# Performance work log

Measured on AMD Instinct MI355X. Metric: run time of the kernel, lower is better.

The kernel has to match this reference:

```python
import jax, jax.numpy as jnp
import numpy as np
import math

B, L, D = 2, 2048, 1024
H = 16
DH = D // H  # 64
XPOS_SCALE_BASE = 512.0
THETA = 10000.0


def setup_inputs() -> dict:
    key = jax.random.key(0)
    ks = jax.random.split(key, 9)
    s = 0.02  # keep logits in a sane range like trained weights
    return {
        "x": jax.random.normal(ks[0], (B, L, D), dtype=jnp.float32),
        "Wq": jax.random.normal(ks[1], (D, D), dtype=jnp.float32) * s,
        "bq": jax.random.normal(ks[2], (D,), dtype=jnp.float32) * s,
        "Wk": jax.random.normal(ks[3], (D, D), dtype=jnp.float32) * s,
        "bk": jax.random.normal(ks[4], (D,), dtype=jnp.float32) * s,
        "Wv": jax.random.normal(ks[5], (D, D), dtype=jnp.float32) * s,
        "bv": jax.random.normal(ks[6], (D,), dtype=jnp.float32) * s,
        "Wo": jax.random.normal(ks[7], (D, D), dtype=jnp.float32) * s,
        "bo": jax.random.normal(ks[8], (D,), dtype=jnp.float32) * s,
    }


def _rotate_half(t):
    # pairwise interleaved rotation, as in rotary_embedding_torch
    t1 = t[..., 0::2]
    t2 = t[..., 1::2]
    return jnp.stack([-t2, t1], axis=-1).reshape(t.shape)


def _xpos_rotate(q, k):
    # q, k: [B, H, L, DH]; xPos rotary embedding (use_xpos=True)
    seq = q.shape[2]
    half = jnp.arange(0, DH, 2, dtype=jnp.float32)
    inv_freq = 1.0 / (THETA ** (half / DH))            # [DH/2]
    t = jnp.arange(seq, dtype=jnp.float32)             # [L]
    freqs = t[:, None] * inv_freq[None, :]             # [L, DH/2]
    freqs = jnp.repeat(freqs, 2, axis=-1)              # [L, DH] interleaved
    # xPos length-extrapolatable scale
    scale_vec = (half + 0.4 * DH) / (1.4 * DH)         # [DH/2]
    power = (t - seq // 2) / XPOS_SCALE_BASE           # [L]
    scale = scale_vec[None, :] ** power[:, None]       # [L, DH/2]
    scale = jnp.repeat(scale, 2, axis=-1)              # [L, DH]
    cos = jnp.cos(freqs)
    sin = jnp.sin(freqs)
    q_out = q * (cos * scale) + _rotate_half(q) * (sin * scale)
    k_out = k * (cos / scale) + _rotate_half(k) * (sin / scale)
    return q_out, k_out


def reference(x, Wq, bq, Wk, bk, Wv, bv, Wo, bo):
    b, l, d = x.shape
    # projections; note source swaps names: v_mat <- k-proj, k_mat <- v-proj
    q = (x @ Wq.T + bq).reshape(b, l, H, DH).transpose(0, 2, 1, 3)  # [b,h,l,dh]
    v = (x @ Wk.T + bk).reshape(b, l, H, DH).transpose(0, 2, 1, 3)
    k = (x @ Wv.T + bv).reshape(b, l, H, DH).transpose(0, 2, 1, 3)
    q, k = _xpos_rotate(q, k)
    # source divides by sqrt(Dh * num_heads) == sqrt(dim)
    scores = jnp.einsum("bhqd,bhkd->bhqk", q, k) / math.sqrt(d)
    weights = jax.nn.softmax(scores, axis=-1)
    inter = jnp.einsum("bhqk,bhkd->bhqd", weights, v)
    inter = inter.transpose(0, 2, 1, 3).reshape(b, l, d)
    return inter @ Wo.T + bo
```

## Files before the change

kernel.cpp:

```cpp
#include <hip/hip_runtime.h>
#include <math.h>

#define NB 2
#define NL 2048
#define ND 1024
#define NH 16
#define NDH 64
#define NBL 4096

typedef __attribute__((ext_vector_type(4)))  float f32x4;
typedef __attribute__((ext_vector_type(16))) float f32x16;
typedef __attribute__((ext_vector_type(8)))  short s16x8;
typedef __attribute__((ext_vector_type(4)))  short s16x4;

#define LOG2E 1.44269504088896f

__device__ __forceinline__ float fexp2(float x){
#if __has_builtin(__builtin_amdgcn_exp2f)
  return __builtin_amdgcn_exp2f(x);
#else
  return exp2f(x);
#endif
}

__device__ __forceinline__ unsigned short f2bf(float f){
  unsigned int u = __float_as_uint(f);
  u += 0x7FFF + ((u >> 16) & 1);
  return (unsigned short)(u >> 16);
}

__device__ __forceinline__ unsigned int pk2bf(float lo, float hi){
  return __builtin_amdgcn_perm(__float_as_uint(hi) + 0x8000u,
                               __float_as_uint(lo) + 0x8000u, 0x07060302u);
}

__global__ void cvt_all(const float* __restrict__ x,
                        const float* __restrict__ wq, const float* __restrict__ wk,
                        const float* __restrict__ wv, const float* __restrict__ wo,
                        unsigned short* __restrict__ xb,
                        unsigned short* __restrict__ wqb, unsigned short* __restrict__ wkb,
                        unsigned short* __restrict__ wvb, unsigned short* __restrict__ wob){
  int i = blockIdx.x * blockDim.x + threadIdx.x;
  const float* s; unsigned short* d; int off;
  if (i < (1<<20)) { s = x; d = xb; off = i; }
  else {
    int j = i - (1<<20); int w = j >> 18; off = j & ((1<<18)-1);
    s = (w==0)?wq:(w==1)?wk:(w==2)?wv:wo;
    d = (w==0)?wqb:(w==1)?wkb:(w==2)?wvb:wob;
  }
  float4 f = reinterpret_cast<const float4*>(s)[off];
  ushort4 r; r.x=f2bf(f.x); r.y=f2bf(f.y); r.z=f2bf(f.z); r.w=f2bf(f.w);
  reinterpret_cast<ushort4*>(d)[off] = r;
}

__global__ void rope_tables(float2* __restrict__ qtab, float2* __restrict__ ktab){
  int t = blockIdx.x * blockDim.x + threadIdx.x;
  int l = t >> 5, i = t & 31;
  float half = 2.0f * (float)i;
  float inv_freq = 1.0f / powf(10000.0f, half / 64.0f);
  float fr = (float)l * inv_freq;
  float sv = (half + 0.4f * 64.0f) / (1.4f * 64.0f);
  float pw = ((float)l - 1024.0f) / 512.0f;
  float sc = powf(sv, pw);
  float cs = cosf(fr), sn = sinf(fr);
  qtab[t] = make_float2(cs * sc, sn * sc);
  ktab[t] = make_float2(cs / sc, sn / sc);
}

__device__ __forceinline__ void gemm_core128(
    const unsigned short* __restrict__ A, const unsigned short* __restrict__ W,
    int row0, int col0,
    unsigned short (&As)[128][32], unsigned short (&Bs)[128][32],
    f32x4 (&acc)[4][4])
{
  const int tid  = threadIdx.x;
  const int wave = tid >> 6, lane = tid & 63;
  const int m16  = lane & 15, quad = lane >> 4;
  const int mrow = (wave & 1) * 64, ncol = (wave >> 1) * 64;
  const int rA   = lane >> 2, cA = (lane & 3) * 8;

  for (int k0 = 0; k0 < ND; k0 += 32){
    __syncthreads();
#pragma unroll
    for (int i2 = 0; i2 < 2; i2++){
      const int c = wave * 2 + i2;
      const unsigned short* ga = A + (size_t)(row0 + c*16 + rA) * ND + k0 + cA;
      const unsigned short* gb = W + (size_t)(col0 + c*16 + rA) * ND + k0 + cA;
      __builtin_amdgcn_global_load_lds((const __attribute__((address_space(1))) void*)ga,
                                       (__attribute__((address_space(3))) void*)&As[c*16][0], 16, 0, 0);
      __builtin_amdgcn_global_load_lds((const __attribute__((address_space(1))) void*)gb,
                                       (__attribute__((address_space(3))) void*)&Bs[c*16][0], 16, 0, 0);
    }
    __syncthreads();
    s16x8 af[4], bf[4];
#pragma unroll
    for (int mt = 0; mt < 4; mt++) af[mt] = *reinterpret_cast<const s16x8*>(&As[mrow + mt*16 + m16][quad*8]);
#pragma unroll
    for (int nt = 0; nt < 4; nt++) bf[nt] = *reinterpret_cast<const s16x8*>(&Bs[ncol + nt*16 + m16][quad*8]);
#pragma unroll
    for (int mt = 0; mt < 4; mt++)
#pragma unroll
      for (int nt = 0; nt < 4; nt++)
        acc[mt][nt] = __builtin_amdgcn_mfma_f32_16x16x32_bf16(af[mt], bf[nt], acc[mt][nt], 0, 0, 0);
  }
}

__global__ __launch_bounds__(256) void gemm_qkv(
    const unsigned short* __restrict__ A,
    const unsigned short* __restrict__ Wq, const float* __restrict__ bq,
    const unsigned short* __restrict__ Wk, const float* __restrict__ bk,
    const unsigned short* __restrict__ Wv, const float* __restrict__ bv,
    unsigned short* __restrict__ qb, unsigned short* __restrict__ kb,
    unsigned short* __restrict__ vtb,
    const float2* __restrict__ qtab, const float2* __restrict__ ktab)
{
  __shared__ unsigned short As[128][32];
  __shared__ unsigned short Bs[128][32];
  __shared__ unsigned short T[128][72];

  const int mode = blockIdx.z;
  const unsigned short* W = (mode==0) ? Wq : (mode==1) ? Wk : Wv;
  const float* bias       = (mode==0) ? bq : (mode==1) ? bk : bv;

  const int row0 = blockIdx.x * 128, col0 = blockIdx.y * 128;
  f32x4 acc[4][4] = {};
  gemm_core128(A, W, row0, col0, As, Bs, acc);

  const int tid  = threadIdx.x;
  const int wave = tid >> 6, lane = tid & 63;
  const int m16  = lane & 15, quad = lane >> 4;
  const int mrow = (wave & 1) * 64, ncol = (wave >> 1) * 64;

  if (mode == 2){
    const int b = row0 >> 11, l0 = row0 & (NL - 1);
#pragma unroll
    for (int h2 = 0; h2 < 2; h2++){
      __syncthreads();
      if ((wave >> 1) == h2){
#pragma unroll
        for (int mt = 0; mt < 4; mt++)
#pragma unroll
          for (int nt = 0; nt < 4; nt++)
#pragma unroll
            for (int r = 0; r < 4; r++){
              int lrow = mrow + mt*16 + quad*4 + r;
              int dh   = nt*16 + m16;
              T[lrow][dh] = f2bf(acc[mt][nt][r] + bias[col0 + h2*64 + dh]);
            }
      }
      __syncthreads();
      const int bh = b * NH + (col0 >> 6) + h2;
#pragma unroll
      for (int j4 = 0; j4 < 4; j4++){
        int c = tid * 4 + j4;
        int d = c >> 4, seg = (c & 15) * 8;
        unsigned short tmp[8];
#pragma unroll
        for (int jj = 0; jj < 8; jj++) tmp[jj] = T[seg + jj][d];
        *reinterpret_cast<uint4*>(vtb + (size_t)(bh * NDH + d) * NL + l0 + seg) =
            *reinterpret_cast<uint4*>(tmp);
      }
    }
  } else {
    const float qscale = (mode == 0) ? (0.03125f * LOG2E) : 1.0f;
    const float2* tab  = (mode == 0) ? qtab : ktab;
    unsigned short* dst = (mode == 0) ? qb : kb;
#pragma unroll
    for (int mt = 0; mt < 4; mt++)
#pragma unroll
      for (int nt = 0; nt < 4; nt++)
#pragma unroll
        for (int r = 0; r < 4; r++){
          int grow = row0 + mrow + mt*16 + quad*4 + r;
          int gcol = col0 + ncol + nt*16 + m16;
          float v = acc[mt][nt][r] + bias[gcol];
          int b = grow >> 11, l = grow & (NL - 1);
          int h = gcol >> 6, dh = gcol & 63;
          float pv = __shfl_xor(v, 1);
          float2 t = tab[l*32 + (dh >> 1)];
          float rh = (dh & 1) ? pv : -pv;
          float ov = (v * t.x + rh * t.y) * qscale;
          dst[(((size_t)(b * NH + h)) * NL + l) * NDH + dh] = f2bf(ov);
        }
  }
}

__global__ __launch_bounds__(256) void gemm_o(
    const unsigned short* __restrict__ A, const unsigned short* __restrict__ W,
    const float* __restrict__ bias, float* __restrict__ out)
{
  __shared__ unsigned short As[128][32];
  __shared__ unsigned short Bs[64][32];
  const int tid  = threadIdx.x;
  const int wave = tid >> 6, lane = tid & 63;
  const int m16  = lane & 15, quad = lane >> 4;
  const int mrow = (wave & 1) * 64, ncol = (wave >> 1) * 32;
  const int rA   = lane >> 2, cA = (lane & 3) * 8;
  const int row0 = blockIdx.x * 128, col0 = blockIdx.y * 64;

  f32x4 acc[4][2] = {};

  for (int k0 = 0; k0 < ND; k0 += 32){
    __syncthreads();
#pragma unroll
    for (int i3 = 0; i3 < 3; i3++){
      const int c = wave * 3 + i3;
      const unsigned short* g; unsigned short* l;
      if (c < 8){ g = A + (size_t)(row0 + c*16 + rA) * ND + k0 + cA;      l = &As[c*16][0]; }
      else      { g = W + (size_t)(col0 + (c-8)*16 + rA) * ND + k0 + cA;  l = &Bs[(c-8)*16][0]; }
      __builtin_amdgcn_global_load_lds((const __attribute__((address_space(1))) void*)g,
                                       (__attribute__((address_space(3))) void*)l, 16, 0, 0);
    }
    __syncthreads();
    s16x8 af[4], bf[2];
#pragma unroll
    for (int mt = 0; mt < 4; mt++) af[mt] = *reinterpret_cast<const s16x8*>(&As[mrow + mt*16 + m16][quad*8]);
#pragma unroll
    for (int nt = 0; nt < 2; nt++) bf[nt] = *reinterpret_cast<const s16x8*>(&Bs[ncol + nt*16 + m16][quad*8]);
#pragma unroll
    for (int mt = 0; mt < 4; mt++)
#pragma unroll
      for (int nt = 0; nt < 2; nt++)
        acc[mt][nt] = __builtin_amdgcn_mfma_f32_16x16x32_bf16(af[mt], bf[nt], acc[mt][nt], 0, 0, 0);
  }

#pragma unroll
  for (int mt = 0; mt < 4; mt++)
#pragma unroll
    for (int nt = 0; nt < 2; nt++)
#pragma unroll
      for (int r = 0; r < 4; r++){
        int grow = row0 + mrow + mt*16 + quad*4 + r;
        int gcol = col0 + ncol + nt*16 + m16;
        out[(size_t)grow * ND + gcol] = acc[mt][nt][r] + bias[gcol];
      }
}

__global__ __launch_bounds__(256, 2) void attn_kernel(
    const unsigned short* __restrict__ qb,
    const unsigned short* __restrict__ kb,
    const unsigned short* __restrict__ vtb,
    unsigned short* __restrict__ ob)
{
  __shared__ unsigned short Ks[64 * 64];
  __shared__ unsigned short Vs[64 * 64];
  __shared__ unsigned short Os[128 * 72];

  const int tid  = threadIdx.x;
  const int wave = tid >> 6, lane = tid & 63;
  const int l31  = lane & 31, g = lane >> 5;
  const int bh   = blockIdx.y;
  const int q0   = blockIdx.x * 128;
  const unsigned short* Q  = qb  + (size_t)bh * NL * NDH;
  const unsigned short* K  = kb  + (size_t)bh * NL * NDH;
  const unsigned short* Vt = vtb + (size_t)bh * NDH * NL;

  s16x8 qf[4];
#pragma unroll
  for (int s = 0; s < 4; s++)
    qf[s] = *reinterpret_cast<const s16x8*>(
        Q + (size_t)(q0 + wave*32 + l31) * NDH + s*16 + g*8);

  const int r0 = tid >> 3,          c0 = tid & 7;
  const int r1 = (tid + 256) >> 3,  c1 = tid & 7;
  unsigned short* ksw0 = &Ks[r0*64 + ((c0 ^ (r0 & 7)) * 8)];
  unsigned short* ksw1 = &Ks[r1*64 + ((c1 ^ (r1 & 7)) * 8)];
  unsigned short* vsw0 = &Vs[r0*64 + ((c0 ^ (r0 & 7)) * 8)];
  unsigned short* vsw1 = &Vs[r1*64 + ((c1 ^ (r1 & 7)) * 8)];

  uint4 kreg0 = *reinterpret_cast<const uint4*>(K  + (size_t)r0 * NDH + c0*8);
  uint4 kreg1 = *reinterpret_cast<const uint4*>(K  + (size_t)r1 * NDH + c1*8);
  uint4 vreg0 = *reinterpret_cast<const uint4*>(Vt + (size_t)r0 * NL  + c0*8);
  uint4 vreg1 = *reinterpret_cast<const uint4*>(Vt + (size_t)r1 * NL  + c1*8);

  float ls = 0.f;
  f32x16 ot[2] = {};

  for (int kt = 0; kt < 32; kt++){
    __syncthreads();
    *reinterpret_cast<uint4*>(ksw0) = kreg0;
    *reinterpret_cast<uint4*>(ksw1) = kreg1;
    *reinterpret_cast<uint4*>(vsw0) = vreg0;
    *reinterpret_cast<uint4*>(vsw1) = vreg1;
    __syncthreads();

    if (kt < 31){
      const int k0n = (kt + 1) * 64;
      kreg0 = *reinterpret_cast<const uint4*>(K  + (size_t)(k0n + r0) * NDH + c0*8);
      kreg1 = *reinterpret_cast<const uint4*>(K  + (size_t)(k0n + r1) * NDH + c1*8);
      vreg0 = *reinterpret_cast<const uint4*>(Vt + (size_t)r0 * NL + k0n + c0*8);
      vreg1 = *reinterpret_cast<const uint4*>(Vt + (size_t)r1 * NL + k0n + c1*8);
    }

    f32x16 st[2] = {};
#pragma unroll
    for (int t = 0; t < 2; t++){
      const int key = t*32 + l31;
#pragma unroll
      for (int s = 0; s < 4; s++){
        const int cg = (2*s + g) ^ (key & 7);
        s16x8 kf = *reinterpret_cast<const s16x8*>(&Ks[key*64 + cg*8]);
        st[t] = __builtin_amdgcn_mfma_f32_32x32x16_bf16(kf, qf[s], st[t], 0, 0, 0);
      }
    }

    unsigned int pe[2][8];
#pragma unroll
    for (int t = 0; t < 2; t++){
#pragma unroll
      for (int i = 0; i < 8; i++){
        float e0 = fexp2(st[t][2*i]);
        float e1 = fexp2(st[t][2*i + 1]);
        ls += e0 + e1;
        pe[t][i] = pk2bf(e0, e1);
      }
    }

#pragma unroll
    for (int mt = 0; mt < 2; mt++){
      const int dh = mt*32 + l31;
#pragma unroll
      for (int s = 0; s < 8; s++){
        const int cg = (s ^ (dh & 7));
        s16x4 vf = *reinterpret_cast<const s16x4*>(&Vs[dh*64 + cg*8 + g*4]);
        uint2 pb; pb.x = pe[s>>2][2*(s&3)]; pb.y = pe[s>>2][2*(s&3)+1];
        s16x4 pf = *reinterpret_cast<const s16x4*>(&pb);
        ot[mt] = __builtin_amdgcn_mfma_f32_32x32x8bf16_1k(vf, pf, ot[mt], 0, 0, 0);
      }
    }
  }

  float lt = ls + __shfl_xor(ls, 32);
  float linv = 1.0f / lt;

#pragma unroll
  for (int mt = 0; mt < 2; mt++){
#pragma unroll
    for (int s = 0; s < 4; s++){
      float o0 = ot[mt][4*s    ] * linv;
      float o1 = ot[mt][4*s + 1] * linv;
      float o2 = ot[mt][4*s + 2] * linv;
      float o3 = ot[mt][4*s + 3] * linv;
      uint2 pk; pk.x = pk2bf(o0, o1); pk.y = pk2bf(o2, o3);
      *reinterpret_cast<uint2*>(&Os[(wave*32 + l31)*72 + mt*32 + s*8 + g*4]) = pk;
    }
  }
  __syncthreads();

  const int bb = bh >> 4, h = bh & 15;
#pragma unroll
  for (int j = 0; j < 4; j++){
    int idx = tid * 4 + j;
    int row = idx >> 3, cg = (idx & 7) * 8;
    *reinterpret_cast<uint4*>(ob + ((size_t)(bb*NL + q0 + row)) * ND + h*NDH + cg) =
        *reinterpret_cast<const uint4*>(&Os[row*72 + cg]);
  }
}

extern "C" void kernel_launch(void* const* d_in, const int* in_sizes, int n_in,
                              void* d_out, int out_size, void* d_ws, size_t ws_size,
                              hipStream_t stream)
{
  (void)in_sizes; (void)n_in; (void)out_size; (void)ws_size;
  const float* x  = (const float*)d_in[0];
  const float* Wq = (const float*)d_in[1];
  const float* bq = (const float*)d_in[2];
  const float* Wk = (const float*)d_in[3];
  const float* bk = (const float*)d_in[4];
  const float* Wv = (const float*)d_in[5];
  const float* bv = (const float*)d_in[6];
  const float* Wo = (const float*)d_in[7];
  const float* bo = (const float*)d_in[8];
  float* out = (float*)d_out;

  char* p = (char*)d_ws;
  unsigned short* xb   = (unsigned short*)p; p += (size_t)NBL*ND*2;
  unsigned short* wqb  = (unsigned short*)p; p += (size_t)ND*ND*2;
  unsigned short* wkb  = (unsigned short*)p; p += (size_t)ND*ND*2;
  unsigned short* wvb  = (unsigned short*)p; p += (size_t)ND*ND*2;
  unsigned short* wob  = (unsigned short*)p; p += (size_t)ND*ND*2;
  unsigned short* qbuf = (unsigned short*)p; p += (size_t)NBL*ND*2;
  unsigned short* kbuf = (unsigned short*)p; p += (size_t)NBL*ND*2;
  unsigned short* vtb  = (unsigned short*)p; p += (size_t)NBL*ND*2;
  unsigned short* ibuf = (unsigned short*)p; p += (size_t)NBL*ND*2;
  float2* qtab = (float2*)p; p += (size_t)NL*32*8;
  float2* ktab = (float2*)p; p += (size_t)NL*32*8;

  hipLaunchKernelGGL(cvt_all, dim3(8192), dim3(256), 0, stream,
                     x, Wq, Wk, Wv, Wo, xb, wqb, wkb, wvb, wob);
  hipLaunchKernelGGL(rope_tables, dim3(NL*32/256), dim3(256), 0, stream, qtab, ktab);

  hipLaunchKernelGGL(gemm_qkv, dim3(NBL/128, ND/128, 3), dim3(256), 0, stream,
                     xb, wqb, bq, wvb, bv, wkb, bk, qbuf, kbuf, vtb, qtab, ktab);

  hipLaunchKernelGGL(attn_kernel, dim3(NL/128, NB*NH), dim3(256), 0, stream,
                     qbuf, kbuf, vtb, ibuf);

  hipLaunchKernelGGL(gemm_o, dim3(NBL/128, ND/64), dim3(256), 0, stream, ibuf, wob, bo, out);
}
```

Measured before the change: 209.3 us.

## Double query rows per wave and double-buffer K/V tiles in attention

Each wave now handles 64 query rows, two 32-row groups, instead of 32. Every K and V fragment read from shared memory feeds two MFMAs, halving LDS traffic and global K/V reloads per query. K/V tiles are double-buffered in a unified shared buffer, cutting two barriers per iteration to one and prefetching two tiles ahead. The grid halves to 256 blocks, launch bounds drop to one block per SIMD set, and register pressure rises, so occupancy and load balance across CUs may suffer.

```diff
diff --git a/kernel.cpp b/kernel.cpp
--- a/kernel.cpp
+++ b/kernel.cpp
@@ -236,83 +236,92 @@
       }
 }
 
-__global__ __launch_bounds__(256, 2) void attn_kernel(
+__global__ __launch_bounds__(256, 1) void attn_kernel(
     const unsigned short* __restrict__ qb,
     const unsigned short* __restrict__ kb,
     const unsigned short* __restrict__ vtb,
     unsigned short* __restrict__ ob)
 {
-  __shared__ unsigned short Ks[64 * 64];
-  __shared__ unsigned short Vs[64 * 64];
-  __shared__ unsigned short Os[128 * 72];
-
+  __shared__ unsigned short smem[256 * 72];
   const int tid  = threadIdx.x;
   const int wave = tid >> 6, lane = tid & 63;
   const int l31  = lane & 31, g = lane >> 5;
   const int bh   = blockIdx.y;
-  const int q0   = blockIdx.x * 128;
+  const int q0   = blockIdx.x * 256;
   const unsigned short* Q  = qb  + (size_t)bh * NL * NDH;
   const unsigned short* K  = kb  + (size_t)bh * NL * NDH;
   const unsigned short* Vt = vtb + (size_t)bh * NDH * NL;
 
-  s16x8 qf[4];
-#pragma unroll
-  for (int s = 0; s < 4; s++)
-    qf[s] = *reinterpret_cast<const s16x8*>(
-        Q + (size_t)(q0 + wave*32 + l31) * NDH + s*16 + g*8);
+  s16x8 qf[2][4];
+#pragma unroll
+  for (int q2 = 0; q2 < 2; q2++)
+#pragma unroll
+    for (int s = 0; s < 4; s++)
+      qf[q2][s] = *reinterpret_cast<const s16x8*>(
+          Q + (size_t)(q0 + wave*64 + q2*32 + l31) * NDH + s*16 + g*8);
 
   const int r0 = tid >> 3,          c0 = tid & 7;
   const int r1 = (tid + 256) >> 3,  c1 = tid & 7;
-  unsigned short* ksw0 = &Ks[r0*64 + ((c0 ^ (r0 & 7)) * 8)];
-  unsigned short* ksw1 = &Ks[r1*64 + ((c1 ^ (r1 & 7)) * 8)];
-  unsigned short* vsw0 = &Vs[r0*64 + ((c0 ^ (r0 & 7)) * 8)];
-  unsigned short* vsw1 = &Vs[r1*64 + ((c1 ^ (r1 & 7)) * 8)];
+  const int so0 = r0*64 + ((c0 ^ (r0 & 7)) * 8);
+  const int so1 = r1*64 + ((c1 ^ (r1 & 7)) * 8);
 
   uint4 kreg0 = *reinterpret_cast<const uint4*>(K  + (size_t)r0 * NDH + c0*8);
   uint4 kreg1 = *reinterpret_cast<const uint4*>(K  + (size_t)r1 * NDH + c1*8);
   uint4 vreg0 = *reinterpret_cast<const uint4*>(Vt + (size_t)r0 * NL  + c0*8);
   uint4 vreg1 = *reinterpret_cast<const uint4*>(Vt + (size_t)r1 * NL  + c1*8);
-
-  float ls = 0.f;
-  f32x16 ot[2] = {};
+  *reinterpret_cast<uint4*>(&smem[so0])         = kreg0;
+  *reinterpret_cast<uint4*>(&smem[so1])         = kreg1;
+  *reinterpret_cast<uint4*>(&smem[8192 + so0])  = vreg0;
+  *reinterpret_cast<uint4*>(&smem[8192 + so1])  = vreg1;
+  kreg0 = *reinterpret_cast<const uint4*>(K  + (size_t)(64 + r0) * NDH + c0*8);
+  kreg1 = *reinterpret_cast<const uint4*>(K  + (size_t)(64 + r1) * NDH + c1*8);
+  vreg0 = *reinterpret_cast<const uint4*>(Vt + (size_t)r0 * NL + 64 + c0*8);
+  vreg1 = *reinterpret_cast<const uint4*>(Vt + (size_t)r1 * NL + 64 + c1*8);
+  __syncthreads();
+
+  float ls[2] = {0.f, 0.f};
+  f32x16 ot[2][2] = {};
+  const int key7 = l31 & 7;
 
   for (int kt = 0; kt < 32; kt++){
-    __syncthreads();
-    *reinterpret_cast<uint4*>(ksw0) = kreg0;
-    *reinterpret_cast<uint4*>(ksw1) = kreg1;
-    *reinterpret_cast<uint4*>(vsw0) = vreg0;
-    *reinterpret_cast<uint4*>(vsw1) = vreg1;
-    __syncthreads();
-
+    const int cur = (kt & 1) * 4096;
+    const int nxt = 4096 - cur;
     if (kt < 31){
-      const int k0n = (kt + 1) * 64;
+      *reinterpret_cast<uint4*>(&smem[nxt + so0])        = kreg0;
+      *reinterpret_cast<uint4*>(&smem[nxt + so1])        = kreg1;
+      *reinterpret_cast<uint4*>(&smem[8192 + nxt + so0]) = vreg0;
+      *reinterpret_cast<uint4*>(&smem[8192 + nxt + so1]) = vreg1;
+    }
+    if (kt < 30){
+      const int k0n = (kt + 2) * 64;
       kreg0 = *reinterpret_cast<const uint4*>(K  + (size_t)(k0n + r0) * NDH + c0*8);
       kreg1 = *reinterpret_cast<const uint4*>(K  + (size_t)(k0n + r1) * NDH + c1*8);
       vreg0 = *reinterpret_cast<const uint4*>(Vt + (size_t)r0 * NL + k0n + c0*8);
       vreg1 = *reinterpret_cast<const uint4*>(Vt + (size_t)r1 * NL + k0n + c1*8);
     }
 
-    f32x16 st[2] = {};
+    const unsigned short* Kb = &smem[cur];
+    const unsigned short* Vb = &smem[8192 + cur];
+
+    unsigned int pe[2][2][8];
 #pragma unroll
     for (int t = 0; t < 2; t++){
-      const int key = t*32 + l31;
+      f32x16 st0 = {}, st1 = {};
 #pragma unroll
       for (int s = 0; s < 4; s++){
-        const int cg = (2*s + g) ^ (key & 7);
-        s16x8 kf = *reinterpret_cast<const s16x8*>(&Ks[key*64 + cg*8]);
-        st[t] = __builtin_amdgcn_mfma_f32_32x32x16_bf16(kf, qf[s], st[t], 0, 0, 0);
-      }
-    }
-
-    unsigned int pe[2][8];
-#pragma unroll
-    for (int t = 0; t < 2; t++){
+        const int cg = (2*s + g) ^ key7;
+        s16x8 kf = *reinterpret_cast<const s16x8*>(&Kb[(t*32 + l31)*64 + cg*8]);
+        st0 = __builtin_amdgcn_mfma_f32_32x32x16_bf16(kf, qf[0][s], st0, 0, 0, 0);
+        st1 = __builtin_amdgcn_mfma_f32_32x32x16_bf16(kf, qf[1][s], st1, 0, 0, 0);
+      }
 #pragma unroll
       for (int i = 0; i < 8; i++){
-        float e0 = fexp2(st[t][2*i]);
-        float e1 = fexp2(st[t][2*i + 1]);
-        ls += e0 + e1;
-        pe[t][i] = pk2bf(e0, e1);
+        float a0 = fexp2(st0[2*i]), a1 = fexp2(st0[2*i+1]);
+        ls[0] += a0 + a1;
+        pe[0][t][i] = pk2bf(a0, a1);
+        float b0 = fexp2(st1[2*i]), b1 = fexp2(st1[2*i+1]);
+        ls[1] += b0 + b1;
+        pe[1][t][i] = pk2bf(b0, b1);
       }
     }
 
@@ -321,39 +330,48 @@
       const int dh = mt*32 + l31;
 #pragma unroll
       for (int s = 0; s < 8; s++){
-        const int cg = (s ^ (dh & 7));
-        s16x4 vf = *reinterpret_cast<const s16x4*>(&Vs[dh*64 + cg*8 + g*4]);
-        uint2 pb; pb.x = pe[s>>2][2*(s&3)]; pb.y = pe[s>>2][2*(s&3)+1];
-        s16x4 pf = *reinterpret_cast<const s16x4*>(&pb);
-        ot[mt] = __builtin_amdgcn_mfma_f32_32x32x8bf16_1k(vf, pf, ot[mt], 0, 0, 0);
-      }
-    }
-  }
-
-  float lt = ls + __shfl_xor(ls, 32);
-  float linv = 1.0f / lt;
-
-#pragma unroll
-  for (int mt = 0; mt < 2; mt++){
-#pragma unroll
-    for (int s = 0; s < 4; s++){
-      float o0 = ot[mt][4*s    ] * linv;
-      float o1 = ot[mt][4*s + 1] * linv;
-      float o2 = ot[mt][4*s + 2] * linv;
-      float o3 = ot[mt][4*s + 3] * linv;
-      uint2 pk; pk.x = pk2bf(o0, o1); pk.y = pk2bf(o2, o3);
-      *reinterpret_cast<uint2*>(&Os[(wave*32 + l31)*72 + mt*32 + s*8 + g*4]) = pk;
-    }
-  }
+        const int cg = s ^ (dh & 7);
+        s16x4 vf = *reinterpret_cast<const s16x4*>(&Vb[dh*64 + cg*8 + g*4]);
+        uint2 pb0; pb0.x = pe[0][s>>2][2*(s&3)]; pb0.y = pe[0][s>>2][2*(s&3)+1];
+        ot[mt][0] = __builtin_amdgcn_mfma_f32_32x32x8bf16_1k(
+            vf, *reinterpret_cast<s16x4*>(&pb0), ot[mt][0], 0, 0, 0);
+        uint2 pb1; pb1.x = pe[1][s>>2][2*(s&3)]; pb1.y = pe[1][s>>2][2*(s&3)+1];
+        ot[mt][1] = __builtin_amdgcn_mfma_f32_32x32x8bf16_1k(
+            vf, *reinterpret_cast<s16x4*>(&pb1), ot[mt][1], 0, 0, 0);
+      }
+    }
+    __syncthreads();
+  }
+
+  float linv[2];
+#pragma unroll
+  for (int q2 = 0; q2 < 2; q2++){
+    float t = ls[q2] + __shfl_xor(ls[q2], 32);
+    linv[q2] = 1.0f / t;
+  }
+
+#pragma unroll
+  for (int mt = 0; mt < 2; mt++)
+#pragma unroll
+    for (int q2 = 0; q2 < 2; q2++)
+#pragma unroll
+      for (int s = 0; s < 4; s++){
+        float o0 = ot[mt][q2][4*s    ] * linv[q2];
+        float o1 = ot[mt][q2][4*s + 1] * linv[q2];
+        float o2 = ot[mt][q2][4*s + 2] * linv[q2];
+        float o3 = ot[mt][q2][4*s + 3] * linv[q2];
+        uint2 pk; pk.x = pk2bf(o0, o1); pk.y = pk2bf(o2, o3);
+        *reinterpret_cast<uint2*>(&smem[(wave*64 + q2*32 + l31)*72 + mt*32 + s*8 + g*4]) = pk;
+      }
   __syncthreads();
 
   const int bb = bh >> 4, h = bh & 15;
 #pragma unroll
-  for (int j = 0; j < 4; j++){
-    int idx = tid * 4 + j;
-    int row = idx >> 3, cg = (idx & 7) * 8;
-    *reinterpret_cast<uint4*>(ob + ((size_t)(bb*NL + q0 + row)) * ND + h*NDH + cg) =
-        *reinterpret_cast<const uint4*>(&Os[row*72 + cg]);
+  for (int j = 0; j < 8; j++){
+    int idx = j*256 + tid;
+    int row = idx >> 3, cg2 = (idx & 7) * 8;
+    *reinterpret_cast<uint4*>(ob + ((size_t)(bb*NL + q0 + row)) * ND + h*NDH + cg2) =
+        *reinterpret_cast<const uint4*>(&smem[row*72 + cg2]);
   }
 }
 
@@ -393,7 +411,7 @@
   hipLaunchKernelGGL(gemm_qkv, dim3(NBL/128, ND/128, 3), dim3(256), 0, stream,
                      xb, wqb, bq, wvb, bv, wkb, bk, qbuf, kbuf, vtb, qtab, ktab);
 
-  hipLaunchKernelGGL(attn_kernel, dim3(NL/128, NB*NH), dim3(256), 0, stream,
+  hipLaunchKernelGGL(attn_kernel, dim3(NL/256, NB*NH), dim3(256), 0, stream,
                      qbuf, kbuf, vtb, ibuf);
 
   hipLaunchKernelGGL(gemm_o, dim3(NBL/128, ND/64), dim3(256), 0, stream, ibuf, wob, bo, out);
```

After: 208.9 us. Within noise of the previous version (-0.2%).
